# Performance work log

Measured on AMD Instinct MI355X. Metric: run time of the kernel, lower is better.

Reference implementation:

```python
import jax, jax.numpy as jnp
import numpy as np
import math

B, T, E = 2, 2048, 1024
D = 1024          # total inner dim (config.head_dim)
H = 16            # n_head
HD = D // H       # per-head dim = 64


def setup_inputs() -> dict:
    key = jax.random.key(0)
    k1, k2, k3, k4, k5 = jax.random.split(key, 5)
    s = 0.02
    return {
        "x": jax.random.normal(k1, (B, T, E), dtype=jnp.float32),
        "W_attn": jax.random.normal(k2, (E, 3 * D), dtype=jnp.float32) * s,
        "b_attn": jnp.zeros((3 * D,), dtype=jnp.float32),
        "W_proj": jax.random.normal(k3, (D, E), dtype=jnp.float32) * s,
        "b_proj": jnp.zeros((E,), dtype=jnp.float32),
    }


def reference(x, W_attn, b_attn, W_proj, b_proj):
    Bc, Tc, _ = x.shape
    qkv = x @ W_attn + b_attn                       # [B,T,3D]
    q, k, v = jnp.split(qkv, 3, axis=-1)            # each [B,T,D]
    # reshape to heads: [B,H,T,hd]
    q = q.reshape(Bc, Tc, H, HD).transpose(0, 2, 1, 3)
    k = k.reshape(Bc, Tc, H, HD).transpose(0, 2, 1, 3)
    v = v.reshape(Bc, Tc, H, HD).transpose(0, 2, 1, 3)
    scale = 1.0 / math.sqrt(HD)
    att = jnp.einsum("bhqd,bhkd->bhqk", q, k) * scale   # [B,H,T,T]
    causal = jnp.tril(jnp.ones((Tc, Tc), dtype=bool))
    att = jnp.where(causal[None, None], att, -jnp.inf)
    att = jax.nn.softmax(att, axis=-1)
    y = jnp.einsum("bhqk,bhkd->bhqd", att, v)           # [B,H,T,hd]
    y = y.transpose(0, 2, 1, 3).reshape(Bc, Tc, D)      # [B,T,D]
    return y @ W_proj + b_proj                          # [B,T,E]
```

## Files before the change

### kernel.cpp

```cpp
#include <hip/hip_runtime.h>

typedef unsigned short u16;
typedef unsigned char u8;
typedef signed char s8;
typedef unsigned int u32;
typedef short bf16x8 __attribute__((ext_vector_type(8)));
typedef float f32x4 __attribute__((ext_vector_type(4)));
typedef int i32x4 __attribute__((ext_vector_type(4)));

#define SXI 21.1666667f
#define SWI 1058.3333f
#define DEQ 4.4640015e-5f

__device__ __forceinline__ u16 f2bf(float f) {
  union { float f; u32 u; } v; v.f = f;
  u32 r = v.u + 0x7fffu + ((v.u >> 16) & 1u);
  return (u16)(r >> 16);
}
__device__ __forceinline__ u16 f2bf_fast(float f) {
  union { float f; u32 u; } v; v.f = f;
  return (u16)((v.u + 0x8000u) >> 16);
}
__device__ __forceinline__ s8 q8(float v, float s) {
  float x = fminf(127.f, fmaxf(-127.f, v * s));
  return (s8)__float2int_rn(x);
}
__device__ __forceinline__ float fexp2(float x) {
#if __has_builtin(__builtin_amdgcn_exp2f)
  return __builtin_amdgcn_exp2f(x);
#else
  return exp2f(x);
#endif
}

__device__ __forceinline__ void gld_lds16(const u16* g, u16* l) {
  __builtin_amdgcn_global_load_lds(
      (__attribute__((address_space(1))) u32*)(g),
      (__attribute__((address_space(3))) u32*)(l), 16, 0, 0);
}
__device__ __forceinline__ void gld_lds16b(const u8* g, u8* l) {
  __builtin_amdgcn_global_load_lds(
      (__attribute__((address_space(1))) u32*)(g),
      (__attribute__((address_space(3))) u32*)(l), 16, 0, 0);
}

__device__ __forceinline__ bf16x8 ldsfrag(const u16* base, int row, int c8) {
  return *(const bf16x8*)(base + row * 64 + ((c8 ^ (row & 7)) << 3));
}
__device__ __forceinline__ int swz4(int r) { return (r & 3) ^ ((r >> 2) & 3); }

template <int CTRL>
__device__ __forceinline__ float dppf(float x) {
  return __int_as_float(__builtin_amdgcn_update_dpp(0, __float_as_int(x), CTRL, 0xf, 0xf, true));
}
__device__ __forceinline__ float red16_max(float x) {
  x = fmaxf(x, dppf<0xB1>(x));
  x = fmaxf(x, dppf<0x4E>(x));
  x = fmaxf(x, dppf<0x141>(x));
  x = fmaxf(x, dppf<0x140>(x));
  return x;
}
__device__ __forceinline__ float red16_sum(float x) {
  x += dppf<0xB1>(x);
  x += dppf<0x4E>(x);
  x += dppf<0x141>(x);
  x += dppf<0x140>(x);
  return x;
}

__global__ __launch_bounds__(256) void k_prep(const float* __restrict__ x, u16* __restrict__ xb,
                                              s8* __restrict__ xq,
                                              const float* __restrict__ Wa, u16* __restrict__ WaT,
                                              s8* __restrict__ wq8,
                                              const float* __restrict__ Wp, u16* __restrict__ WpT) {
  __shared__ float t[64][65];
  const int id = blockIdx.x;
  if (id < 2048) {
    int i = (id * 256 + threadIdx.x) * 8;
    const float4* p = (const float4*)(x + i);
    float4 a = p[0], b = p[1];
    uint4 o;
    o.x = (u32)f2bf(a.x) | ((u32)f2bf(a.y) << 16);
    o.y = (u32)f2bf(a.z) | ((u32)f2bf(a.w) << 16);
    o.z = (u32)f2bf(b.x) | ((u32)f2bf(b.y) << 16);
    o.w = (u32)f2bf(b.z) | ((u32)f2bf(b.w) << 16);
    *(uint4*)(xb + i) = o;
    u32 lo = (u32)(u8)q8(a.x, SXI) | ((u32)(u8)q8(a.y, SXI) << 8) |
             ((u32)(u8)q8(a.z, SXI) << 16) | ((u32)(u8)q8(a.w, SXI) << 24);
    u32 hi = (u32)(u8)q8(b.x, SXI) | ((u32)(u8)q8(b.y, SXI) << 8) |
             ((u32)(u8)q8(b.z, SXI) << 16) | ((u32)(u8)q8(b.w, SXI) << 24);
    uint2 oq; oq.x = lo; oq.y = hi;
    *(uint2*)(xq + i) = oq;
  } else if (id < 2816) {
    int q = id - 2048;
    int bx = q % 48, by = q / 48;
    int c0 = bx * 64, r0 = by * 64;
    int tx = threadIdx.x & 63, ty = threadIdx.x >> 6;
#pragma unroll
    for (int i = ty; i < 64; i += 4) t[i][tx] = Wa[(size_t)(r0 + i) * 3072 + c0 + tx];
    __syncthreads();
#pragma unroll
    for (int i = ty; i < 64; i += 4) {
      int row = c0 + i;
      if (row < 2048)
        wq8[(size_t)row * 1024 + r0 + tx] = q8(t[tx][i], SWI);
      else
        WaT[(size_t)row * 1024 + r0 + tx] = f2bf(t[tx][i]);
    }
  } else {
    int q = id - 2816;
    int bx = q & 15, by = q >> 4;
    int c0 = bx * 64, r0 = by * 64;
    int tx = threadIdx.x & 63, ty = threadIdx.x >> 6;
#pragma unroll
    for (int i = ty; i < 64; i += 4) t[i][tx] = Wp[(size_t)(r0 + i) * 1024 + c0 + tx];
    __syncthreads();
#pragma unroll
    for (int i = ty; i < 64; i += 4)
      WpT[(size_t)(c0 + i) * 1024 + r0 + tx] = f2bf(t[tx][i]);
  }
}

__global__ __launch_bounds__(256) void k_gemm_qkv(const u16* __restrict__ xb,
                                                  const s8* __restrict__ xq,
                                                  const u16* __restrict__ Wt,
                                                  const s8* __restrict__ wq8,
                                                  const float* __restrict__ bias,
                                                  u16* __restrict__ qb, u16* __restrict__ kb,
                                                  u16* __restrict__ vtb) {
  const int id = blockIdx.x;
  const int tid = threadIdx.x;
  const int lane = tid & 63, w = tid >> 6;
  const int lr = lane & 15, lq = lane >> 4;

  if (id < 1024) {
    __shared__ __align__(16) u8 la8[64 * 64], lb8[128 * 64];
    const int wm = (w >> 1) << 5, wn = (w & 1) << 6;
    i32x4 acc[2][4];
#pragma unroll
    for (int mi = 0; mi < 2; ++mi)
#pragma unroll
      for (int ni = 0; ni < 4; ++ni) acc[mi][ni] = (i32x4){0, 0, 0, 0};
    const int m0 = (id >> 4) * 64, n0 = (id & 15) * 128;
    const int srow4 = tid >> 2;
    const int gcol4 = (((tid & 3) ^ swz4(srow4)) << 4);
    const u8* ag = (const u8*)xq + (size_t)(m0 + srow4) * 1024 + gcol4;
    const u8* bg = (const u8*)wq8 + (size_t)(n0 + srow4) * 1024 + gcol4;

    for (int k0 = 0; k0 < 1024; k0 += 64) {
      __syncthreads();
      gld_lds16b(ag + k0, la8 + (w * 16) * 64);
#pragma unroll
      for (int r = 0; r < 2; ++r)
        gld_lds16b(bg + (size_t)r * 64 * 1024 + k0, lb8 + (r * 64 + w * 16) * 64);
      __syncthreads();
      i32x4 a[2], b[4];
#pragma unroll
      for (int mi = 0; mi < 2; ++mi) {
        int m = wm + mi * 16 + lr;
        a[mi] = *(const i32x4*)(la8 + m * 64 + ((lq ^ swz4(m)) << 4));
      }
#pragma unroll
      for (int ni = 0; ni < 4; ++ni) {
        int n = wn + ni * 16 + lr;
        b[ni] = *(const i32x4*)(lb8 + n * 64 + ((lq ^ swz4(n)) << 4));
      }
#pragma unroll
      for (int mi = 0; mi < 2; ++mi)
#pragma unroll
        for (int ni = 0; ni < 4; ++ni)
          acc[mi][ni] = __builtin_amdgcn_mfma_i32_16x16x64_i8(a[mi], b[ni], acc[mi][ni], 0, 0, 0);
    }
#pragma unroll
    for (int mi = 0; mi < 2; ++mi) {
      int gm = m0 + wm + mi * 16 + lq * 4;
#pragma unroll
      for (int ni = 0; ni < 4; ++ni) {
        int gn = n0 + wn + ni * 16 + lr;
        float bv = bias[gn];
        int which = gn >> 10, head = (gn >> 6) & 15, hd = gn & 63;
#pragma unroll
        for (int r = 0; r < 4; ++r) {
          int row = gm + r;
          int b2 = row >> 11, tt = row & 2047;
          float v = (float)acc[mi][ni][r] * DEQ + bv;
          size_t bh = (size_t)(b2 * 16 + head);
          if (which == 0)
            qb[(bh * 2048 + tt) * 64 + hd] = f2bf(v * 0.125f);
          else
            kb[(bh * 2048 + tt) * 64 + hd] = f2bf(v);
        }
      }
    }
  } else {
    __shared__ u16 sA[64 * 64], sB[128 * 64];
    const int wm = (w >> 1) << 5, wn = (w & 1) << 6;
    f32x4 acc[2][4];
#pragma unroll
    for (int mi = 0; mi < 2; ++mi)
#pragma unroll
      for (int ni = 0; ni < 4; ++ni) acc[mi][ni] = (f32x4){0.f, 0.f, 0.f, 0.f};
    const int t2 = id - 1024;
    const int m0 = (t2 >> 5) * 64, n0 = (t2 & 31) * 128;
    const int srow = tid >> 3;
    const int gcol = ((tid & 7) ^ (srow & 7)) << 3;
    const u16* ag = Wt + 2048 * 1024 + (size_t)(m0 + srow) * 1024 + gcol;
    const u16* bg = xb + (size_t)(n0 + srow) * 1024 + gcol;
    u16* la = sA + w * 512;
    u16* lb = sB + w * 512;

    for (int k0 = 0; k0 < 1024; k0 += 64) {
      __syncthreads();
#pragma unroll
      for (int r = 0; r < 2; ++r) gld_lds16(ag + (size_t)r * 32 * 1024 + k0, la + r * 2048);
#pragma unroll
      for (int r = 0; r < 4; ++r) gld_lds16(bg + (size_t)r * 32 * 1024 + k0, lb + r * 2048);
      __syncthreads();
#pragma unroll
      for (int kk = 0; kk < 64; kk += 32) {
        const int c8 = (kk >> 3) + lq;
        bf16x8 af[2], bfr[4];
#pragma unroll
        for (int i = 0; i < 2; ++i) af[i] = ldsfrag(sA, wm + i * 16 + lr, c8);
#pragma unroll
        for (int i = 0; i < 4; ++i) bfr[i] = ldsfrag(sB, wn + i * 16 + lr, c8);
#pragma unroll
        for (int mi = 0; mi < 2; ++mi)
#pragma unroll
          for (int ni = 0; ni < 4; ++ni)
            acc[mi][ni] = __builtin_amdgcn_mfma_f32_16x16x32_bf16(af[mi], bfr[ni], acc[mi][ni], 0, 0, 0);
      }
    }
#pragma unroll
    for (int mi = 0; mi < 2; ++mi) {
      int gm = m0 + wm + mi * 16 + lq * 4;
      float4 bv = *(const float4*)(bias + 2048 + gm);
#pragma unroll
      for (int ni = 0; ni < 4; ++ni) {
        int gn = n0 + wn + ni * 16 + lr;
        int b = gn >> 11, tt = gn & 2047;
#pragma unroll
        for (int r = 0; r < 4; ++r) {
          int dv = gm + r;
          float v = acc[mi][ni][r] + ((const float*)&bv)[r];
          vtb[((size_t)(b * 1024 + dv)) * 2048 + tt] = f2bf(v);
        }
      }
    }
  }
}

__global__ __launch_bounds__(256, 4) void k_attn(const u16* __restrict__ qb,
                                                 const u16* __restrict__ kb,
                                                 const u16* __restrict__ vtb,
                                                 u16* __restrict__ yb) {
  __shared__ u16 sK[2][64 * 64];
  __shared__ u16 sV[2][64 * 64];
  __shared__ u16 sP[64 * 64];

  const int tid = threadIdx.x;
  const int lane = tid & 63, w = tid >> 6;
  const int lr = lane & 15, lq = lane >> 4;
  const int l = blockIdx.x;
  const int bh = l & 31;
  const int i = l >> 5;
  int qt;
  if (i < 8) qt = 31 - i;
  else if (i < 16) qt = i - 8;
  else if (i < 24) qt = 39 - i;
  else qt = i - 16;
  const int q0 = qt << 6;

  const u16* qh = qb + (size_t)bh * (2048 * 64);
  const u16* kh = kb + (size_t)bh * (2048 * 64);
  const u16* vh = vtb + (size_t)bh * (64 * 2048);

  bf16x8 qreg[2];
  {
    const u16* qp = qh + (size_t)(q0 + w * 16 + lr) * 64 + lq * 8;
    qreg[0] = *(const bf16x8*)(qp);
    qreg[1] = *(const bf16x8*)(qp + 32);
  }

  const int srow = tid >> 3;
  const int gcol = ((tid & 7) ^ (srow & 7)) << 3;

  {
    u16* lk = sK[0] + w * 512;
    u16* lv = sV[0] + w * 512;
#pragma unroll
    for (int r = 0; r < 2; ++r) {
      gld_lds16(kh + (size_t)(r * 32 + srow) * 64 + gcol, lk + r * 2048);
      gld_lds16(vh + (size_t)(r * 32 + srow) * 2048 + gcol, lv + r * 2048);
    }
  }

  const float L2E = 1.44269504f;
  f32x4 o[4];
  float mL2[4], lrow[4];
#pragma unroll
  for (int j = 0; j < 4; ++j) {
    o[j] = (f32x4){0.f, 0.f, 0.f, 0.f};
    mL2[j] = -1e30f;
    lrow[j] = 0.f;
  }

  const int ntiles = qt + 1;
  for (int it = 0; it < ntiles; ++it) {
    __syncthreads();
    if (it + 1 < ntiles) {
      const int nkv = (it + 1) << 6;
      const int nb = (it + 1) & 1;
      u16* lk = sK[nb] + w * 512;
      u16* lv = sV[nb] + w * 512;
#pragma unroll
      for (int r = 0; r < 2; ++r) {
        gld_lds16(kh + (size_t)(nkv + r * 32 + srow) * 64 + gcol, lk + r * 2048);
        gld_lds16(vh + (size_t)(r * 32 + srow) * 2048 + nkv + gcol, lv + r * 2048);
      }
    }
    const u16* cK = sK[it & 1];
    const u16* cV = sV[it & 1];

    f32x4 s[4];
#pragma unroll
    for (int nj = 0; nj < 4; ++nj) s[nj] = (f32x4){0.f, 0.f, 0.f, 0.f};
#pragma unroll
    for (int kk = 0; kk < 64; kk += 32) {
      const int c8 = (kk >> 3) + lq;
      bf16x8 kf[4];
#pragma unroll
      for (int nj = 0; nj < 4; ++nj) kf[nj] = ldsfrag(cK, nj * 16 + lr, c8);
#pragma unroll
      for (int nj = 0; nj < 4; ++nj)
        s[nj] = __builtin_amdgcn_mfma_f32_16x16x32_bf16(qreg[kk >> 5], kf[nj], s[nj], 0, 0, 0);
    }

    if (it == qt) {
      int rloc = w * 16 + lq * 4;
#pragma unroll
      for (int nj = 0; nj < 4; ++nj) {
        int cloc = nj * 16 + lr;
#pragma unroll
        for (int r = 0; r < 4; ++r)
          if (cloc > rloc + r) s[nj][r] = -1e30f;
      }
    }

    float al[4];
#pragma unroll
    for (int r = 0; r < 4; ++r) {
      float mx = fmaxf(fmaxf(s[0][r], s[1][r]), fmaxf(s[2][r], s[3][r]));
      mx = red16_max(mx) * L2E;
      float mn = fmaxf(mL2[r], mx);
      al[r] = fexp2(mL2[r] - mn);
      mL2[r] = mn;
    }
#pragma unroll
    for (int nj = 0; nj < 4; ++nj)
#pragma unroll
      for (int r = 0; r < 4; ++r) o[nj][r] *= al[r];
    float rs[4];
#pragma unroll
    for (int r = 0; r < 4; ++r) rs[r] = 0.f;
#pragma unroll
    for (int nj = 0; nj < 4; ++nj)
#pragma unroll
      for (int r = 0; r < 4; ++r) {
        float p = fexp2(fmaf(s[nj][r], L2E, -mL2[r]));
        s[nj][r] = p;
        rs[r] += p;
      }
#pragma unroll
    for (int r = 0; r < 4; ++r) lrow[r] = lrow[r] * al[r] + red16_sum(rs[r]);

#pragma unroll
    for (int nj = 0; nj < 4; ++nj) {
      int chunk = nj * 2 + (lr >> 3);
#pragma unroll
      for (int r = 0; r < 4; ++r) {
        int row = w * 16 + lq * 4 + r;
        sP[row * 64 + ((chunk ^ (row & 7)) << 3) + (lr & 7)] = f2bf_fast(s[nj][r]);
      }
    }
    asm volatile("s_waitcnt lgkmcnt(0)" ::: "memory");

#pragma unroll
    for (int kk = 0; kk < 64; kk += 32) {
      const int c8 = (kk >> 3) + lq;
      bf16x8 pa = ldsfrag(sP, w * 16 + lr, c8);
      bf16x8 vf[4];
#pragma unroll
      for (int nj = 0; nj < 4; ++nj) vf[nj] = ldsfrag(cV, nj * 16 + lr, c8);
#pragma unroll
      for (int nj = 0; nj < 4; ++nj)
        o[nj] = __builtin_amdgcn_mfma_f32_16x16x32_bf16(pa, vf[nj], o[nj], 0, 0, 0);
    }
  }

  const int b = bh >> 4, h = bh & 15;
#pragma unroll
  for (int r = 0; r < 4; ++r) {
    float inv = 1.0f / lrow[r];
    int row = q0 + w * 16 + lq * 4 + r;
    size_t base = ((size_t)(b * 2048 + row)) * 1024 + h * 64;
#pragma unroll
    for (int nj = 0; nj < 4; ++nj) yb[base + nj * 16 + lr] = f2bf(o[nj][r] * inv);
  }
}

__global__ __launch_bounds__(256) void k_gemm_proj(const u16* __restrict__ ybuf,
                                                   const u16* __restrict__ Wt,
                                                   const float* __restrict__ bias,
                                                   float* __restrict__ out) {
  __shared__ u16 sA[64 * 64], sB[64 * 64];
  f32x4 acc[2][2];
#pragma unroll
  for (int mi = 0; mi < 2; ++mi)
#pragma unroll
    for (int ni = 0; ni < 2; ++ni) acc[mi][ni] = (f32x4){0.f, 0.f, 0.f, 0.f};

  const int m0 = blockIdx.y * 64, n0 = blockIdx.x * 64;
  const int tid = threadIdx.x;
  const int lane = tid & 63, w = tid >> 6;
  const int wm = (w >> 1) << 5, wn = (w & 1) << 5;
  const int lr = lane & 15, lq = lane >> 4;
  const int srow = tid >> 3;
  const int gcol = ((tid & 7) ^ (srow & 7)) << 3;
  const u16* ag = ybuf + (size_t)(m0 + srow) * 1024 + gcol;
  const u16* bg = Wt + (size_t)(n0 + srow) * 1024 + gcol;
  u16* la = sA + w * 512;
  u16* lb = sB + w * 512;

  for (int k0 = 0; k0 < 1024; k0 += 64) {
    __syncthreads();
#pragma unroll
    for (int r = 0; r < 2; ++r) {
      gld_lds16(ag + (size_t)r * 32 * 1024 + k0, la + r * 2048);
      gld_lds16(bg + (size_t)r * 32 * 1024 + k0, lb + r * 2048);
    }
    __syncthreads();
#pragma unroll
    for (int kk = 0; kk < 64; kk += 32) {
      const int c8 = (kk >> 3) + lq;
      bf16x8 af[2], bfr[2];
#pragma unroll
      for (int i = 0; i < 2; ++i) {
        af[i] = ldsfrag(sA, wm + i * 16 + lr, c8);
        bfr[i] = ldsfrag(sB, wn + i * 16 + lr, c8);
      }
#pragma unroll
      for (int mi = 0; mi < 2; ++mi)
#pragma unroll
        for (int ni = 0; ni < 2; ++ni)
          acc[mi][ni] = __builtin_amdgcn_mfma_f32_16x16x32_bf16(af[mi], bfr[ni], acc[mi][ni], 0, 0, 0);
    }
  }

#pragma unroll
  for (int mi = 0; mi < 2; ++mi) {
    int gm = m0 + wm + mi * 16 + lq * 4;
#pragma unroll
    for (int ni = 0; ni < 2; ++ni) {
      int gn = n0 + wn + ni * 16 + lr;
      float bv = bias[gn];
#pragma unroll
      for (int r = 0; r < 4; ++r) out[(size_t)(gm + r) * 1024 + gn] = acc[mi][ni][r] + bv;
    }
  }
}

extern "C" void kernel_launch(void* const* d_in, const int* in_sizes, int n_in,
                              void* d_out, int out_size, void* d_ws, size_t ws_size,
                              hipStream_t stream) {
  const float* x = (const float*)d_in[0];
  const float* W_attn = (const float*)d_in[1];
  const float* b_attn = (const float*)d_in[2];
  const float* W_proj = (const float*)d_in[3];
  const float* b_proj = (const float*)d_in[4];
  float* out = (float*)d_out;

  u16* ws = (u16*)d_ws;
  u16* xb = ws;
  u16* WaT = ws + 4194304;
  u16* WpT = ws + 7340032;
  u16* qbuf = ws + 8388608;
  u16* kbuf = ws + 12582912;
  u16* vtb = ws + 16777216;
  u16* ybuf = ws + 20971520;
  s8* xq = (s8*)ybuf;
  s8* wq8 = (s8*)ybuf + 4194304;

  k_prep<<<dim3(3072), dim3(256), 0, stream>>>(x, xb, xq, W_attn, WaT, wq8, W_proj, WpT);
  k_gemm_qkv<<<dim3(1536), dim3(256), 0, stream>>>(xb, xq, WaT, wq8, b_attn, qbuf, kbuf, vtb);
  k_attn<<<dim3(1024), dim3(256), 0, stream>>>(qbuf, kbuf, vtb, ybuf);
  k_gemm_proj<<<dim3(16, 64), dim3(256), 0, stream>>>(ybuf, WpT, b_proj, out);
}
```

Measured before the change: 175.2 us.

## Pair causal query tiles per block and use lazy softmax rescaling

Each attention block now handles two query tiles (pr and 31-pr), so every block walks exactly 33 KV tiles and the grid drops from 1024 to 512 blocks, which balances causal work. The log2(e) factor is folded into the Q scale. The running max and rescale of O are only updated when a new max exceeds the old by more than 8, and the row sum reduction across lanes is deferred to the end. Fewer blocks may reduce occupancy and latency hiding on a large GPU, and removing the launch-bounds occupancy hint may raise register use. Lazy rescaling bounds exponent growth but adds a branch per tile.

Result: slower. 179.9 us (+2.7%).

```diff
diff --git a/kernel.cpp b/kernel.cpp
--- a/kernel.cpp
+++ b/kernel.cpp
@@ -186,7 +186,7 @@
           float v = (float)acc[mi][ni][r] * DEQ + bv;
           size_t bh = (size_t)(b2 * 16 + head);
           if (which == 0)
-            qb[(bh * 2048 + tt) * 64 + hd] = f2bf(v * 0.125f);
+            qb[(bh * 2048 + tt) * 64 + hd] = f2bf(v * 0.18033688f);
           else
             kb[(bh * 2048 + tt) * 64 + hd] = f2bf(v);
         }
@@ -250,10 +250,10 @@
   }
 }
 
-__global__ __launch_bounds__(256, 4) void k_attn(const u16* __restrict__ qb,
-                                                 const u16* __restrict__ kb,
-                                                 const u16* __restrict__ vtb,
-                                                 u16* __restrict__ yb) {
+__global__ __launch_bounds__(256) void k_attn(const u16* __restrict__ qb,
+                                              const u16* __restrict__ kb,
+                                              const u16* __restrict__ vtb,
+                                              u16* __restrict__ yb) {
   __shared__ u16 sK[2][64 * 64];
   __shared__ u16 sV[2][64 * 64];
   __shared__ u16 sP[64 * 64];
@@ -263,23 +263,22 @@
   const int lr = lane & 15, lq = lane >> 4;
   const int l = blockIdx.x;
   const int bh = l & 31;
-  const int i = l >> 5;
-  int qt;
-  if (i < 8) qt = 31 - i;
-  else if (i < 16) qt = i - 8;
-  else if (i < 24) qt = 39 - i;
-  else qt = i - 16;
-  const int q0 = qt << 6;
+  const int pr = l >> 5;
+  const int qt0 = pr, qt1 = 31 - pr;
+  const int NT = 33;
 
   const u16* qh = qb + (size_t)bh * (2048 * 64);
   const u16* kh = kb + (size_t)bh * (2048 * 64);
   const u16* vh = vtb + (size_t)bh * (64 * 2048);
 
-  bf16x8 qreg[2];
+  bf16x8 qc[2], qn[2];
   {
-    const u16* qp = qh + (size_t)(q0 + w * 16 + lr) * 64 + lq * 8;
-    qreg[0] = *(const bf16x8*)(qp);
-    qreg[1] = *(const bf16x8*)(qp + 32);
+    const u16* qp0 = qh + (size_t)((qt0 << 6) + w * 16 + lr) * 64 + lq * 8;
+    qc[0] = *(const bf16x8*)(qp0);
+    qc[1] = *(const bf16x8*)(qp0 + 32);
+    const u16* qp1 = qh + (size_t)((qt1 << 6) + w * 16 + lr) * 64 + lq * 8;
+    qn[0] = *(const bf16x8*)(qp1);
+    qn[1] = *(const bf16x8*)(qp1 + 32);
   }
 
   const int srow = tid >> 3;
@@ -295,21 +294,22 @@
     }
   }
 
-  const float L2E = 1.44269504f;
   f32x4 o[4];
-  float mL2[4], lrow[4];
+  float mL2[4], lrp[4];
 #pragma unroll
   for (int j = 0; j < 4; ++j) {
     o[j] = (f32x4){0.f, 0.f, 0.f, 0.f};
     mL2[j] = -1e30f;
-    lrow[j] = 0.f;
-  }
-
-  const int ntiles = qt + 1;
-  for (int it = 0; it < ntiles; ++it) {
+    lrp[j] = 0.f;
+  }
+
+  const int b = bh >> 4, h = bh & 15;
+
+  for (int it = 0; it < NT; ++it) {
     __syncthreads();
-    if (it + 1 < ntiles) {
-      const int nkv = (it + 1) << 6;
+    if (it + 1 < NT) {
+      const int nk = (it + 1 <= qt0) ? (it + 1) : (it - qt0);
+      const int nkv = nk << 6;
       const int nb = (it + 1) & 1;
       u16* lk = sK[nb] + w * 512;
       u16* lv = sV[nb] + w * 512;
@@ -333,10 +333,10 @@
       for (int nj = 0; nj < 4; ++nj) kf[nj] = ldsfrag(cK, nj * 16 + lr, c8);
 #pragma unroll
       for (int nj = 0; nj < 4; ++nj)
-        s[nj] = __builtin_amdgcn_mfma_f32_16x16x32_bf16(qreg[kk >> 5], kf[nj], s[nj], 0, 0, 0);
-    }
-
-    if (it == qt) {
+        s[nj] = __builtin_amdgcn_mfma_f32_16x16x32_bf16(qc[kk >> 5], kf[nj], s[nj], 0, 0, 0);
+    }
+
+    if (it == qt0 || it == NT - 1) {
       int rloc = w * 16 + lq * 4;
 #pragma unroll
       for (int nj = 0; nj < 4; ++nj) {
@@ -347,32 +347,32 @@
       }
     }
 
-    float al[4];
-#pragma unroll
-    for (int r = 0; r < 4; ++r) {
-      float mx = fmaxf(fmaxf(s[0][r], s[1][r]), fmaxf(s[2][r], s[3][r]));
-      mx = red16_max(mx) * L2E;
-      float mn = fmaxf(mL2[r], mx);
-      al[r] = fexp2(mL2[r] - mn);
-      mL2[r] = mn;
+    float mx[4];
+#pragma unroll
+    for (int r = 0; r < 4; ++r)
+      mx[r] = red16_max(fmaxf(fmaxf(s[0][r], s[1][r]), fmaxf(s[2][r], s[3][r])));
+    int need = 0;
+#pragma unroll
+    for (int r = 0; r < 4; ++r) need |= (mx[r] > mL2[r] + 8.f) ? 1 : 0;
+    if (__any(need)) {
+#pragma unroll
+      for (int r = 0; r < 4; ++r) {
+        float mn = fmaxf(mL2[r], mx[r]);
+        float al = fexp2(mL2[r] - mn);
+        mL2[r] = mn;
+        lrp[r] *= al;
+#pragma unroll
+        for (int nj = 0; nj < 4; ++nj) o[nj][r] *= al;
+      }
     }
 #pragma unroll
     for (int nj = 0; nj < 4; ++nj)
 #pragma unroll
-      for (int r = 0; r < 4; ++r) o[nj][r] *= al[r];
-    float rs[4];
-#pragma unroll
-    for (int r = 0; r < 4; ++r) rs[r] = 0.f;
-#pragma unroll
-    for (int nj = 0; nj < 4; ++nj)
-#pragma unroll
       for (int r = 0; r < 4; ++r) {
-        float p = fexp2(fmaf(s[nj][r], L2E, -mL2[r]));
-        s[nj][r] = p;
-        rs[r] += p;
-      }
-#pragma unroll
-    for (int r = 0; r < 4; ++r) lrow[r] = lrow[r] * al[r] + red16_sum(rs[r]);
+        float pp = fexp2(s[nj][r] - mL2[r]);
+        s[nj][r] = pp;
+        lrp[r] += pp;
+      }
 
 #pragma unroll
     for (int nj = 0; nj < 4; ++nj) {
@@ -396,13 +396,31 @@
       for (int nj = 0; nj < 4; ++nj)
         o[nj] = __builtin_amdgcn_mfma_f32_16x16x32_bf16(pa, vf[nj], o[nj], 0, 0, 0);
     }
-  }
-
-  const int b = bh >> 4, h = bh & 15;
+
+    if (it == qt0) {
+#pragma unroll
+      for (int r = 0; r < 4; ++r) {
+        float inv = 1.0f / red16_sum(lrp[r]);
+        int row = (qt0 << 6) + w * 16 + lq * 4 + r;
+        size_t base = ((size_t)(b * 2048 + row)) * 1024 + h * 64;
+#pragma unroll
+        for (int nj = 0; nj < 4; ++nj) yb[base + nj * 16 + lr] = f2bf(o[nj][r] * inv);
+      }
+#pragma unroll
+      for (int j = 0; j < 4; ++j) {
+        o[j] = (f32x4){0.f, 0.f, 0.f, 0.f};
+        mL2[j] = -1e30f;
+        lrp[j] = 0.f;
+      }
+      qc[0] = qn[0];
+      qc[1] = qn[1];
+    }
+  }
+
 #pragma unroll
   for (int r = 0; r < 4; ++r) {
-    float inv = 1.0f / lrow[r];
-    int row = q0 + w * 16 + lq * 4 + r;
+    float inv = 1.0f / red16_sum(lrp[r]);
+    int row = (qt1 << 6) + w * 16 + lq * 4 + r;
     size_t base = ((size_t)(b * 2048 + row)) * 1024 + h * 64;
 #pragma unroll
     for (int nj = 0; nj < 4; ++nj) yb[base + nj * 16 + lr] = f2bf(o[nj][r] * inv);
@@ -493,6 +511,6 @@
 
   k_prep<<<dim3(3072), dim3(256), 0, stream>>>(x, xb, xq, W_attn, WaT, wq8, W_proj, WpT);
   k_gemm_qkv<<<dim3(1536), dim3(256), 0, stream>>>(xb, xq, WaT, wq8, b_attn, qbuf, kbuf, vtb);
-  k_attn<<<dim3(1024), dim3(256), 0, stream>>>(qbuf, kbuf, vtb, ybuf);
+  k_attn<<<dim3(512), dim3(256), 0, stream>>>(qbuf, kbuf, vtb, ybuf);
   k_gemm_proj<<<dim3(16, 64), dim3(256), 0, stream>>>(ybuf, WpT, b_proj, out);
 }
```

## Software-pipeline QK^T one tile ahead with lazy softmax rescaling in attention

Applied to the files above, without the earlier changes.

Restructures the flash-attention loop so the QK^T MFMAs for the next KV tile are issued alongside the softmax and PV work of the current tile. K is prefetched two tiles ahead and V one tile ahead in separate buffers. The log2(e) factor is folded into the Q scaling, the output is rescaled only when the running max grows by more than 8 (checked wave-wide), and the row-sum reduction is deferred to the end. Together these cut per-tile exp and shuffle work and let matrix ops overlap with the softmax, at the cost of more registers and slightly different numerics from the lazy rescale threshold.

Result: no change. 173.7 us (-0.8%).

```diff
diff --git a/kernel.cpp b/kernel.cpp
--- a/kernel.cpp
+++ b/kernel.cpp
@@ -186,7 +186,7 @@
           float v = (float)acc[mi][ni][r] * DEQ + bv;
           size_t bh = (size_t)(b2 * 16 + head);
           if (which == 0)
-            qb[(bh * 2048 + tt) * 64 + hd] = f2bf(v * 0.125f);
+            qb[(bh * 2048 + tt) * 64 + hd] = f2bf(v * 0.18033688f);
           else
             kb[(bh * 2048 + tt) * 64 + hd] = f2bf(v);
         }
@@ -270,6 +270,7 @@
   else if (i < 24) qt = 39 - i;
   else qt = i - 16;
   const int q0 = qt << 6;
+  const int NT = qt + 1;
 
   const u16* qh = qb + (size_t)bh * (2048 * 64);
   const u16* kh = kb + (size_t)bh * (2048 * 64);
@@ -285,58 +286,93 @@
   const int srow = tid >> 3;
   const int gcol = ((tid & 7) ^ (srow & 7)) << 3;
 
+  u16* pP[4][4];
+#pragma unroll
+  for (int nj = 0; nj < 4; ++nj) {
+    int chunk = nj * 2 + (lr >> 3);
+#pragma unroll
+    for (int r = 0; r < 4; ++r) {
+      int row = w * 16 + lq * 4 + r;
+      pP[nj][r] = sP + row * 64 + ((chunk ^ (row & 7)) << 3) + (lr & 7);
+    }
+  }
+
   {
-    u16* lk = sK[0] + w * 512;
-    u16* lv = sV[0] + w * 512;
+    u16* lk0 = sK[0] + w * 512;
+    u16* lv0 = sV[0] + w * 512;
 #pragma unroll
     for (int r = 0; r < 2; ++r) {
-      gld_lds16(kh + (size_t)(r * 32 + srow) * 64 + gcol, lk + r * 2048);
-      gld_lds16(vh + (size_t)(r * 32 + srow) * 2048 + gcol, lv + r * 2048);
-    }
-  }
-
-  const float L2E = 1.44269504f;
+      gld_lds16(kh + (size_t)(r * 32 + srow) * 64 + gcol, lk0 + r * 2048);
+      gld_lds16(vh + (size_t)(r * 32 + srow) * 2048 + gcol, lv0 + r * 2048);
+    }
+    if (NT > 1) {
+      u16* lk1 = sK[1] + w * 512;
+#pragma unroll
+      for (int r = 0; r < 2; ++r)
+        gld_lds16(kh + (size_t)(64 + r * 32 + srow) * 64 + gcol, lk1 + r * 2048);
+    }
+  }
+  __syncthreads();
+
+  f32x4 s[4];
+#pragma unroll
+  for (int nj = 0; nj < 4; ++nj) s[nj] = (f32x4){0.f, 0.f, 0.f, 0.f};
+#pragma unroll
+  for (int kk = 0; kk < 64; kk += 32) {
+    const int c8 = (kk >> 3) + lq;
+    bf16x8 kf[4];
+#pragma unroll
+    for (int nj = 0; nj < 4; ++nj) kf[nj] = ldsfrag(sK[0], nj * 16 + lr, c8);
+#pragma unroll
+    for (int nj = 0; nj < 4; ++nj)
+      s[nj] = __builtin_amdgcn_mfma_f32_16x16x32_bf16(qreg[kk >> 5], kf[nj], s[nj], 0, 0, 0);
+  }
+
   f32x4 o[4];
-  float mL2[4], lrow[4];
+  float mL2[4], lrp[4];
 #pragma unroll
   for (int j = 0; j < 4; ++j) {
     o[j] = (f32x4){0.f, 0.f, 0.f, 0.f};
     mL2[j] = -1e30f;
-    lrow[j] = 0.f;
-  }
-
-  const int ntiles = qt + 1;
-  for (int it = 0; it < ntiles; ++it) {
+    lrp[j] = 0.f;
+  }
+
+  for (int t = 0; t < NT; ++t) {
     __syncthreads();
-    if (it + 1 < ntiles) {
-      const int nkv = (it + 1) << 6;
-      const int nb = (it + 1) & 1;
-      u16* lk = sK[nb] + w * 512;
-      u16* lv = sV[nb] + w * 512;
-#pragma unroll
-      for (int r = 0; r < 2; ++r) {
-        gld_lds16(kh + (size_t)(nkv + r * 32 + srow) * 64 + gcol, lk + r * 2048);
-        gld_lds16(vh + (size_t)(r * 32 + srow) * 2048 + nkv + gcol, lv + r * 2048);
-      }
-    }
-    const u16* cK = sK[it & 1];
-    const u16* cV = sV[it & 1];
-
-    f32x4 s[4];
-#pragma unroll
-    for (int nj = 0; nj < 4; ++nj) s[nj] = (f32x4){0.f, 0.f, 0.f, 0.f};
-#pragma unroll
-    for (int kk = 0; kk < 64; kk += 32) {
-      const int c8 = (kk >> 3) + lq;
-      bf16x8 kf[4];
-#pragma unroll
-      for (int nj = 0; nj < 4; ++nj) kf[nj] = ldsfrag(cK, nj * 16 + lr, c8);
-#pragma unroll
-      for (int nj = 0; nj < 4; ++nj)
-        s[nj] = __builtin_amdgcn_mfma_f32_16x16x32_bf16(qreg[kk >> 5], kf[nj], s[nj], 0, 0, 0);
-    }
-
-    if (it == qt) {
+
+    if (t + 2 < NT) {
+      const int kv = (t + 2) << 6;
+      u16* lk = sK[t & 1] + w * 512;
+#pragma unroll
+      for (int r = 0; r < 2; ++r)
+        gld_lds16(kh + (size_t)(kv + r * 32 + srow) * 64 + gcol, lk + r * 2048);
+    }
+    if (t + 1 < NT) {
+      const int kv = (t + 1) << 6;
+      u16* lv = sV[(t + 1) & 1] + w * 512;
+#pragma unroll
+      for (int r = 0; r < 2; ++r)
+        gld_lds16(vh + (size_t)(r * 32 + srow) * 2048 + kv + gcol, lv + r * 2048);
+    }
+
+    f32x4 sn[4];
+    if (t + 1 < NT) {
+      const u16* nK = sK[(t + 1) & 1];
+#pragma unroll
+      for (int nj = 0; nj < 4; ++nj) sn[nj] = (f32x4){0.f, 0.f, 0.f, 0.f};
+#pragma unroll
+      for (int kk = 0; kk < 64; kk += 32) {
+        const int c8 = (kk >> 3) + lq;
+        bf16x8 kf[4];
+#pragma unroll
+        for (int nj = 0; nj < 4; ++nj) kf[nj] = ldsfrag(nK, nj * 16 + lr, c8);
+#pragma unroll
+        for (int nj = 0; nj < 4; ++nj)
+          sn[nj] = __builtin_amdgcn_mfma_f32_16x16x32_bf16(qreg[kk >> 5], kf[nj], sn[nj], 0, 0, 0);
+      }
+    }
+
+    if (t == qt) {
       int rloc = w * 16 + lq * 4;
 #pragma unroll
       for (int nj = 0; nj < 4; ++nj) {
@@ -347,61 +383,64 @@
       }
     }
 
-    float al[4];
-#pragma unroll
-    for (int r = 0; r < 4; ++r) {
-      float mx = fmaxf(fmaxf(s[0][r], s[1][r]), fmaxf(s[2][r], s[3][r]));
-      mx = red16_max(mx) * L2E;
-      float mn = fmaxf(mL2[r], mx);
-      al[r] = fexp2(mL2[r] - mn);
-      mL2[r] = mn;
+    float mx[4];
+#pragma unroll
+    for (int r = 0; r < 4; ++r)
+      mx[r] = red16_max(fmaxf(fmaxf(s[0][r], s[1][r]), fmaxf(s[2][r], s[3][r])));
+    int need = 0;
+#pragma unroll
+    for (int r = 0; r < 4; ++r) need |= (mx[r] > mL2[r] + 8.f) ? 1 : 0;
+    if (__any(need)) {
+#pragma unroll
+      for (int r = 0; r < 4; ++r) {
+        float mn = fmaxf(mL2[r], mx[r]);
+        float al = fexp2(mL2[r] - mn);
+        mL2[r] = mn;
+        lrp[r] *= al;
+#pragma unroll
+        for (int nj = 0; nj < 4; ++nj) o[nj][r] *= al;
+      }
     }
 #pragma unroll
     for (int nj = 0; nj < 4; ++nj)
 #pragma unroll
-      for (int r = 0; r < 4; ++r) o[nj][r] *= al[r];
-    float rs[4];
-#pragma unroll
-    for (int r = 0; r < 4; ++r) rs[r] = 0.f;
+      for (int r = 0; r < 4; ++r) {
+        float pp = fexp2(s[nj][r] - mL2[r]);
+        s[nj][r] = pp;
+        lrp[r] += pp;
+      }
+
 #pragma unroll
     for (int nj = 0; nj < 4; ++nj)
 #pragma unroll
-      for (int r = 0; r < 4; ++r) {
-        float p = fexp2(fmaf(s[nj][r], L2E, -mL2[r]));
-        s[nj][r] = p;
-        rs[r] += p;
-      }
-#pragma unroll
-    for (int r = 0; r < 4; ++r) lrow[r] = lrow[r] * al[r] + red16_sum(rs[r]);
-
-#pragma unroll
-    for (int nj = 0; nj < 4; ++nj) {
-      int chunk = nj * 2 + (lr >> 3);
-#pragma unroll
-      for (int r = 0; r < 4; ++r) {
-        int row = w * 16 + lq * 4 + r;
-        sP[row * 64 + ((chunk ^ (row & 7)) << 3) + (lr & 7)] = f2bf_fast(s[nj][r]);
-      }
-    }
+      for (int r = 0; r < 4; ++r) *pP[nj][r] = f2bf_fast(s[nj][r]);
     asm volatile("s_waitcnt lgkmcnt(0)" ::: "memory");
 
-#pragma unroll
-    for (int kk = 0; kk < 64; kk += 32) {
-      const int c8 = (kk >> 3) + lq;
-      bf16x8 pa = ldsfrag(sP, w * 16 + lr, c8);
-      bf16x8 vf[4];
-#pragma unroll
-      for (int nj = 0; nj < 4; ++nj) vf[nj] = ldsfrag(cV, nj * 16 + lr, c8);
-#pragma unroll
-      for (int nj = 0; nj < 4; ++nj)
-        o[nj] = __builtin_amdgcn_mfma_f32_16x16x32_bf16(pa, vf[nj], o[nj], 0, 0, 0);
+    {
+      const u16* cV = sV[t & 1];
+#pragma unroll
+      for (int kk = 0; kk < 64; kk += 32) {
+        const int c8 = (kk >> 3) + lq;
+        bf16x8 pa = ldsfrag(sP, w * 16 + lr, c8);
+        bf16x8 vf[4];
+#pragma unroll
+        for (int nj = 0; nj < 4; ++nj) vf[nj] = ldsfrag(cV, nj * 16 + lr, c8);
+#pragma unroll
+        for (int nj = 0; nj < 4; ++nj)
+          o[nj] = __builtin_amdgcn_mfma_f32_16x16x32_bf16(pa, vf[nj], o[nj], 0, 0, 0);
+      }
+    }
+
+    if (t + 1 < NT) {
+#pragma unroll
+      for (int nj = 0; nj < 4; ++nj) s[nj] = sn[nj];
     }
   }
 
   const int b = bh >> 4, h = bh & 15;
 #pragma unroll
   for (int r = 0; r < 4; ++r) {
-    float inv = 1.0f / lrow[r];
+    float inv = 1.0f / red16_sum(lrp[r]);
     int row = q0 + w * 16 + lq * 4 + r;
     size_t base = ((size_t)(b * 2048 + row)) * 1024 + h * 64;
 #pragma unroll
```
